# Kernel optimization log

Measured on AMD Instinct MI355X. Metric: run time of the kernel, lower is better.

Reference implementation:

```python
import jax, jax.numpy as jnp
import numpy as np

N = 100000
E = 1600000
D = 128          # in_feat == hidden_size
L = 3            # hidden layers
EPS = 1e-5       # BatchNorm1d eps


def setup_inputs() -> dict:
    key = jax.random.key(0)
    ks = jax.random.split(key, 12)
    x = jax.random.normal(ks[0], (N, D), dtype=jnp.float32)
    edge_index = jax.random.randint(ks[1], (2, E), 0, N, dtype=jnp.int64)
    s = 1.0 / np.sqrt(D)
    # stacked hidden-layer SAGEConv params: lin_l (neighbor), lin_r (root), bias on lin_l
    Wl = jax.random.uniform(ks[2], (L, D, D), jnp.float32, -s, s)
    Wr = jax.random.uniform(ks[3], (L, D, D), jnp.float32, -s, s)
    b = jax.random.uniform(ks[4], (L, D), jnp.float32, -s, s)
    # batchnorm affine params
    gamma = jnp.ones((L, D), jnp.float32)
    beta = jnp.zeros((L, D), jnp.float32)
    # output SAGEConv: D -> 1
    Wl_out = jax.random.uniform(ks[5], (D, 1), jnp.float32, -s, s)
    Wr_out = jax.random.uniform(ks[6], (D, 1), jnp.float32, -s, s)
    b_out = jax.random.uniform(ks[7], (1,), jnp.float32, -s, s)
    return {"x": x, "edge_index": edge_index, "Wl": Wl, "Wr": Wr, "b": b,
            "gamma": gamma, "beta": beta, "Wl_out": Wl_out, "Wr_out": Wr_out,
            "b_out": b_out}


def _sage(x, src, dst, inv_deg, Wl, Wr, b):
    # gather neighbor features along edges, mean-aggregate at destination
    msg_sum = jax.ops.segment_sum(x[src], dst, num_segments=N)   # [N, F]
    mean = msg_sum * inv_deg                                     # 0 for isolated nodes
    return mean @ Wl + x @ Wr + b


def _batchnorm(x, gamma, beta):
    m = jnp.mean(x, axis=0)
    v = jnp.mean((x - m) ** 2, axis=0)  # biased var, as torch BN uses for normalization
    return gamma * (x - m) * jax.lax.rsqrt(v + EPS) + beta


def reference(x, edge_index, Wl, Wr, b, gamma, beta, Wl_out, Wr_out, b_out):
    src, dst = edge_index[0], edge_index[1]
    deg = jax.ops.segment_sum(jnp.ones((E,), x.dtype), dst, num_segments=N)
    inv_deg = jnp.where(deg > 0, 1.0 / jnp.maximum(deg, 1.0), 0.0)[:, None]
    h = x
    for i in range(L):
        h = _sage(h, src, dst, inv_deg, Wl[i], Wr[i], b[i])
        h = jax.nn.relu(h)
        h = _batchnorm(h, gamma[i], beta[i])
    out = _sage(h, src, dst, inv_deg, Wl_out, Wr_out, b_out)
    return jax.nn.sigmoid(out)  # [N, 1]
```

## Files before the change

kernel.cpp:

```cpp
#include <hip/hip_runtime.h>

typedef unsigned short u16;
typedef unsigned int u32;
typedef unsigned long long u64;

#define GN 100000
#define GE 1600000
#define DCAP 64
#define NRANGE 196
#define NBKT (NRANGE * 8)
#define BCAP 1536

typedef __bf16 bf16x8 __attribute__((ext_vector_type(8)));
typedef float f32x4 __attribute__((ext_vector_type(4)));
typedef float f32x2 __attribute__((ext_vector_type(2)));
typedef u32 u32x4 __attribute__((ext_vector_type(4)));
typedef u32 u32x2 __attribute__((ext_vector_type(2)));

__device__ __forceinline__ float bl(u32 u){ return __uint_as_float(u << 16); }
__device__ __forceinline__ float bh(u32 u){ return __uint_as_float(u & 0xffff0000u); }
__device__ __forceinline__ float bfu(u16 v){ return __uint_as_float(((u32)v) << 16); }
__device__ __forceinline__ u16 f2bf(float f){
    u32 u = __float_as_uint(f);
    u32 r = (u + 0x7fffu + ((u >> 16) & 1u)) >> 16;
    return (u16)r;
}
__device__ __forceinline__ u32 pack2(float a, float b){
    return (u32)f2bf(a) | ((u32)f2bf(b) << 16);
}
__device__ __forceinline__ u32 pk8x4(float a, float b, float c, float d){
    u32 p = (u32)__builtin_amdgcn_cvt_pk_fp8_f32(a, b, 0, false);
    p = (u32)__builtin_amdgcn_cvt_pk_fp8_f32(c, d, p, true);
    return p;
}

__global__ void __launch_bounds__(256) k_init(const int* ei, const u32* xraw,
                                              int* cursor, float* colpart, int* flags,
                                              int* bcur){
    int i = blockIdx.x * 256 + threadIdx.x;
    if (i < GN) cursor[i] = 0;
    if (i < NBKT) bcur[i] = 0;
    if (i < 6144) colpart[i] = 0.f;
    int t = threadIdx.x;
    if (blockIdx.x == 0){
        __shared__ int s_any[4];
        int v = 0;
        #pragma unroll
        for (int j = 0; j < 4; ++j){
            int k = t * 4 + j;
            v |= ei[2 * k * 1000 + 1];
        }
        #pragma unroll
        for (int m = 1; m < 64; m <<= 1) v |= __shfl_xor(v, m);
        if ((t & 63) == 0) s_any[t >> 6] = v;
        __syncthreads();
        if (t == 0){
            int any = s_any[0] | s_any[1] | s_any[2] | s_any[3];
            flags[0] = (any == 0) ? 1 : 0;
        }
    }
    if (blockIdx.x == 1){
        __shared__ int s_cnt[4];
        int cnt = 0;
        #pragma unroll
        for (int j = 0; j < 4; ++j){
            int idx = (t * 4 + j) * 6000 + 3;
            u32 u = xraw[idx];
            int e = (u >> 7) & 0xFF;
            cnt += (e >= 100 && e <= 140) ? 1 : 0;
        }
        #pragma unroll
        for (int m = 1; m < 64; m <<= 1) cnt += __shfl_xor(cnt, m);
        if ((t & 63) == 0) s_cnt[t >> 6] = cnt;
        __syncthreads();
        if (t == 0){
            int tot = s_cnt[0] + s_cnt[1] + s_cnt[2] + s_cnt[3];
            flags[1] = (tot > 512) ? 0 : 1;
        }
    }
}

__global__ void __launch_bounds__(256) k_convx(const void* x, const int* flags,
                                               u16* xb, u32* h8){
    int gid = blockIdx.x * 256 + threadIdx.x;
    if (gid >= GN * 16) return;
    float f0,f1,f2,f3,f4,f5,f6,f7;
    if (flags[1]){
        const u32x4* xf = (const u32x4*)x;
        u32x4 a = __builtin_nontemporal_load(xf + gid * 2);
        u32x4 b = __builtin_nontemporal_load(xf + gid * 2 + 1);
        f0 = __uint_as_float(a.x); f1 = __uint_as_float(a.y);
        f2 = __uint_as_float(a.z); f3 = __uint_as_float(a.w);
        f4 = __uint_as_float(b.x); f5 = __uint_as_float(b.y);
        f6 = __uint_as_float(b.z); f7 = __uint_as_float(b.w);
    } else {
        u32x4 g = __builtin_nontemporal_load((const u32x4*)x + gid);
        f0 = bl(g.x); f1 = bh(g.x); f2 = bl(g.y); f3 = bh(g.y);
        f4 = bl(g.z); f5 = bh(g.z); f6 = bl(g.w); f7 = bh(g.w);
    }
    u32x4 o;
    o.x = pack2(f0, f1); o.y = pack2(f2, f3);
    o.z = pack2(f4, f5); o.w = pack2(f6, f7);
    ((u32x4*)xb)[gid] = o;
    u32x2 e = { pk8x4(f0, f1, f2, f3), pk8x4(f4, f5, f6, f7) };
    ((u32x2*)h8)[gid] = e;
}

__global__ void __launch_bounds__(256) k_tofp8(const u16* h, u32* h8){
    int gid = blockIdx.x * 256 + threadIdx.x;
    if (gid >= GN * 16) return;
    u32x4 g = ((const u32x4*)h)[gid];
    u32x2 e = { pk8x4(bl(g.x), bh(g.x), bl(g.y), bh(g.y)),
                pk8x4(bl(g.z), bh(g.z), bl(g.w), bh(g.w)) };
    ((u32x2*)h8)[gid] = e;
}

#define WOFF_WR    49152
#define WOFF_B     98304
#define WOFF_G     98688
#define WOFF_BE    99072
#define WOFF_WLO   99456
#define WOFF_WRO   99584
#define WOFF_BO    99712
#define WTOT       99713
__global__ void __launch_bounds__(256) k_convw(const void* Wl, const void* Wr, const void* b,
                                               const void* g, const void* be, const void* wlo,
                                               const void* wro, const void* bo,
                                               const int* flags, u16* wbuf, float* biasf){
    int i = blockIdx.x * 256 + threadIdx.x;
    if (i >= WTOT) return;
    const void* s; int k;
    if (i < WOFF_B){
        const void* src = (i < WOFF_WR) ? Wl : Wr;
        int r = (i < WOFF_WR) ? i : i - WOFF_WR;
        int layer = r >> 14, L = r & 16383;
        int kk = ((L >> 10) << 3) | (L & 7);
        int cc = (L >> 3) & 127;
        int si = layer * 16384 + kk * 128 + cc;
        float fv = flags[1] ? ((const float*)src)[si] : bfu(((const u16*)src)[si]);
        wbuf[i] = f2bf(fv);
        return;
    }
    if      (i < WOFF_G  ){ s = b;   k = i - WOFF_B; }
    else if (i < WOFF_BE ){ s = g;   k = i - WOFF_G; }
    else if (i < WOFF_WLO){ s = be;  k = i - WOFF_BE; }
    else if (i < WOFF_WRO){ s = wlo; k = i - WOFF_WLO; }
    else if (i < WOFF_BO ){ s = wro; k = i - WOFF_WRO; }
    else                  { s = bo;  k = 0; }
    float fv = flags[1] ? ((const float*)s)[k] : bfu(((const u16*)s)[k]);
    wbuf[i] = f2bf(fv);
    if (i >= WOFF_B && i < WOFF_B + 384) biasf[i - WOFF_B] = fv;
}

__global__ void __launch_bounds__(256) k_fillA(const int* ei, const int* flags,
                                               int* bcur, u64* pairs){
    __shared__ int cnt[256];
    __shared__ int lofs[256];
    __shared__ int gbase[NRANGE];
    __shared__ int wsum[4];
    __shared__ u64 lp[1024];
    int t = threadIdx.x;
    int lane = t & 63, w = t >> 6;
    int res = blockIdx.x & 7;
    int base = blockIdx.x * 1024;
    int is64 = flags[0];
    cnt[t] = 0;
    __syncthreads();
    int myd[4], mys[4], slot[4], myr[4];
    #pragma unroll
    for (int j = 0; j < 4; ++j){
        int e = base + j * 256 + t;
        if (e < GE){
            int d, s;
            if (is64){ d = __builtin_nontemporal_load(ei + 2 * (GE + e));
                       s = __builtin_nontemporal_load(ei + 2 * e); }
            else     { d = __builtin_nontemporal_load(ei + GE + e);
                       s = __builtin_nontemporal_load(ei + e); }
            myd[j] = d; mys[j] = s; myr[j] = d >> 9;
            slot[j] = atomicAdd(&cnt[myr[j]], 1);
        } else myr[j] = -1;
    }
    __syncthreads();
    int v = cnt[t];
    int sv = v;
    #pragma unroll
    for (int d = 1; d < 64; d <<= 1){
        int u = __shfl_up(sv, d);
        if (lane >= d) sv += u;
    }
    if (lane == 63) wsum[w] = sv;
    __syncthreads();
    int prefix = 0;
    #pragma unroll
    for (int j = 0; j < 4; ++j) if (j < w) prefix += wsum[j];
    lofs[t] = sv + prefix - v;
    if (t < NRANGE && cnt[t] > 0)
        gbase[t] = atomicAdd(&bcur[t * 8 + res], cnt[t]);
    __syncthreads();
    #pragma unroll
    for (int j = 0; j < 4; ++j){
        if (myr[j] >= 0)
            lp[lofs[myr[j]] + slot[j]] = ((u64)(u32)myd[j] << 32) | (u32)mys[j];
    }
    __syncthreads();
    int total = GE - base; if (total > 1024) total = 1024;
    for (int i = t; i < total; i += 256){
        u64 pr = lp[i];
        int r = (int)(pr >> 32) >> 9;
        int g = gbase[r] + (i - lofs[r]);
        if (g < BCAP) pairs[((size_t)(r * 8 + res)) * BCAP + g] = pr;
    }
}

__global__ void __launch_bounds__(256) k_fillB(const int* bcur, const u64* pairs,
                                               int* cursor, int* col){
    int range = blockIdx.x % 200;
    int sub   = blockIdx.x / 200;
    if (range >= NRANGE || sub >= 8) return;
    int bkt = range * 8 + sub;
    int n = bcur[bkt]; if (n > BCAP) n = BCAP;
    const u64* P = pairs + (size_t)bkt * BCAP;
    for (int i = threadIdx.x; i < n; i += 256){
        u64 pr = __builtin_nontemporal_load(P + i);
        int s = (int)(u32)pr, d = (int)(pr >> 32);
        int pos = atomicAdd(&cursor[d], 1);
        if (pos < DCAP) col[d * DCAP + pos] = s;
    }
}

__global__ void __launch_bounds__(64) k_agg(const u32* h8, const int* deg, const int* col,
                                            u16* amean){
    int lane = threadIdx.x;
    int grp = lane >> 4;
    int lg  = lane & 15;
    int node = blockIdx.x * 4 + grp;
    if (node >= GN) return;
    int d = deg[node];
    int cnt = d < DCAP ? d : DCAP;
    const int* nb = col + node * DCAP;
    const u32x2* hrow = (const u32x2*)h8;
    f32x2 A01 = {0.f, 0.f}, A23 = {0.f, 0.f}, A45 = {0.f, 0.f}, A67 = {0.f, 0.f};
    int e = 0;
    #define ACC8(v) { \
        A01 += __builtin_amdgcn_cvt_pk_f32_fp8((v).x, false); \
        A23 += __builtin_amdgcn_cvt_pk_f32_fp8((v).x, true);  \
        A45 += __builtin_amdgcn_cvt_pk_f32_fp8((v).y, false); \
        A67 += __builtin_amdgcn_cvt_pk_f32_fp8((v).y, true); }
    for (; e + 7 < cnt; e += 8){
        u32x2 v0 = hrow[(size_t)nb[e]     * 16 + lg];
        u32x2 v1 = hrow[(size_t)nb[e + 1] * 16 + lg];
        u32x2 v2 = hrow[(size_t)nb[e + 2] * 16 + lg];
        u32x2 v3 = hrow[(size_t)nb[e + 3] * 16 + lg];
        u32x2 v4 = hrow[(size_t)nb[e + 4] * 16 + lg];
        u32x2 v5 = hrow[(size_t)nb[e + 5] * 16 + lg];
        u32x2 v6 = hrow[(size_t)nb[e + 6] * 16 + lg];
        u32x2 v7 = hrow[(size_t)nb[e + 7] * 16 + lg];
        ACC8(v0) ACC8(v1) ACC8(v2) ACC8(v3) ACC8(v4) ACC8(v5) ACC8(v6) ACC8(v7)
    }
    for (; e + 1 < cnt; e += 2){
        u32x2 v0 = hrow[(size_t)nb[e]     * 16 + lg];
        u32x2 v1 = hrow[(size_t)nb[e + 1] * 16 + lg];
        ACC8(v0) ACC8(v1)
    }
    if (e < cnt){
        u32x2 v0 = hrow[(size_t)nb[e] * 16 + lg];
        ACC8(v0)
    }
    #undef ACC8
    float inv = (d > 0) ? 1.f / (float)d : 0.f;
    f32x2 iv = {inv, inv};
    A01 *= iv; A23 *= iv; A45 *= iv; A67 *= iv;
    u32x4 o;
    o.x = pack2(A01.x, A01.y);
    o.y = pack2(A23.x, A23.y);
    o.z = pack2(A45.x, A45.y);
    o.w = pack2(A67.x, A67.y);
    ((u32x4*)amean)[(size_t)node * 16 + lg] = o;
}

__global__ void __launch_bounds__(256, 4) k_gemm(const u16* amean, const u16* hin,
                                                 const u16* Wlp, const u16* Wrp,
                                                 const float* biasf,
                                                 u16* hout, float* colpart){
    __shared__ float sst[256];
    int t = threadIdx.x;
    int wid = t >> 6, lane = t & 63;
    int quad = lane >> 4, l15 = lane & 15;
    int r0 = blockIdx.x * 128 + wid * 32;
    int node0 = r0 + l15, node1 = r0 + 16 + l15;
    sst[t] = 0.f;

    f32x4 acc[2][8];
    #pragma unroll
    for (int i = 0; i < 2; i++)
        #pragma unroll
        for (int j = 0; j < 8; j++) acc[i][j] = (f32x4){0.f, 0.f, 0.f, 0.f};

    #pragma unroll
    for (int half = 0; half < 2; ++half){
        const u16* A = half ? hin : amean;
        const u32x4* Wg = (const u32x4*)(half ? Wrp : Wlp);
        #pragma unroll
        for (int s = 0; s < 4; ++s){
            int kk = (s << 5) + (quad << 3);
            union { u32x4 u; bf16x8 v; } fa0, fa1;
            fa0.u = (node0 < GN) ? *(const u32x4*)(A + node0 * 128 + kk) : (u32x4){0,0,0,0};
            fa1.u = (node1 < GN) ? *(const u32x4*)(A + node1 * 128 + kk) : (u32x4){0,0,0,0};
            int kc = (s << 2) + quad;
            const u32x4* wg = Wg + (kc << 7) + l15;
            #pragma unroll
            for (int cb = 0; cb < 8; ++cb){
                union { u32x4 u; bf16x8 v; } fw;
                fw.u = wg[cb << 4];
                acc[0][cb] = __builtin_amdgcn_mfma_f32_16x16x32_bf16(fa0.v, fw.v, acc[0][cb], 0, 0, 0);
                acc[1][cb] = __builtin_amdgcn_mfma_f32_16x16x32_bf16(fa1.v, fw.v, acc[1][cb], 0, 0, 0);
            }
        }
    }
    __syncthreads();

    float bsv[8];
    #pragma unroll
    for (int cb = 0; cb < 8; cb++) bsv[cb] = biasf[cb * 16 + l15];

    #pragma unroll
    for (int cb = 0; cb < 8; cb++){
        float csum = 0.f, csq = 0.f;
        #pragma unroll
        for (int rb = 0; rb < 2; rb++){
            int rbase = r0 + rb * 16 + quad * 4;
            #pragma unroll
            for (int rr = 0; rr < 4; rr++){
                int row = rbase + rr;
                float v = acc[rb][cb][rr] + bsv[cb];
                v = fmaxf(v, 0.f);
                if (row < GN) hout[row * 128 + cb * 16 + l15] = f2bf(v);
                float vm = (row < GN) ? v : 0.f;
                csum += vm; csq += vm * vm;
            }
        }
        csum += __shfl_xor(csum, 16); csum += __shfl_xor(csum, 32);
        csq  += __shfl_xor(csq, 16);  csq  += __shfl_xor(csq, 32);
        if (quad == 0){
            atomicAdd(&sst[cb * 16 + l15], csum);
            atomicAdd(&sst[128 + cb * 16 + l15], csq);
        }
    }
    __syncthreads();
    atomicAdd(&colpart[(blockIdx.x & 7) * 256 + t], sst[t]);
}

__global__ void __launch_bounds__(256) k_bnf(const float* colpart, const u16* gamma, const u16* beta,
                                             int mode,
                                             const u16* WlN, const u16* WrN, u16* wfd,
                                             const float* bNsrc, float* bNdst,
                                             const u16* wlo, const u16* wro, const u16* bo,
                                             u16* hwl, u16* hwr, float* hb){
    __shared__ float s_sc[128], s_sh[128], s_red[256];
    int t = threadIdx.x, b = blockIdx.x;
    if (t < 128){
        float s = 0.f, q = 0.f;
        #pragma unroll
        for (int j = 0; j < 8; ++j){
            s += colpart[j * 256 + t];
            q += colpart[j * 256 + 128 + t];
        }
        const float invn = 1.f / (float)GN;
        float mean = s * invn;
        float var = fmaxf(q * invn - mean * mean, 0.f);
        float rstd = rsqrtf(var + 1e-5f);
        float g  = bfu(gamma[t]);
        float be = bfu(beta[t]);
        float sc = g * rstd, sh = be - mean * sc;
        s_sc[t] = sc; s_sh[t] = sh;
    }
    __syncthreads();
    if (mode == 0){
        if (b < 64){
            int idx = b * 256 + t;
            int k = ((idx >> 10) << 3) | (idx & 7);
            float sc = s_sc[k];
            wfd[idx]         = f2bf(sc * bfu(WlN[idx]));
            wfd[16384 + idx] = f2bf(sc * bfu(WrN[idx]));
        } else if (t < 128){
            float acc = bNsrc[t];
            for (int k = 0; k < 128; ++k){
                int L = ((k >> 3) << 10) + (t << 3) + (k & 7);
                acc += s_sh[k] * (bfu(WlN[L]) + bfu(WrN[L]));
            }
            bNdst[t] = acc;
        }
    } else if (b == 64){
        float contrib = 0.f;
        if (t < 128){
            float wl = bfu(wlo[t]), wr = bfu(wro[t]);
            hwl[t] = f2bf(s_sc[t] * wl);
            hwr[t] = f2bf(s_sc[t] * wr);
            contrib = s_sh[t] * (wl + wr);
        }
        s_red[t] = contrib;
        __syncthreads();
        for (int off = 128; off >= 1; off >>= 1){
            if (t < off) s_red[t] += s_red[t + off];
            __syncthreads();
        }
        if (t == 0) hb[0] = s_red[0] + bfu(bo[0]);
    }
}

__global__ void __launch_bounds__(256) k_dot(const u16* h, const u16* wl, const u16* wr,
                                             float* y, float* r){
    int node = (blockIdx.x * 256 + threadIdx.x) >> 6;
    int lane = threadIdx.x & 63;
    if (node >= GN) return;
    u32 hv  = ((const u32*)h)[node * 64 + lane];
    u32 wlv = ((const u32*)wl)[lane];
    u32 wrv = ((const u32*)wr)[lane];
    float hlo = bl(hv), hhi = bh(hv);
    float ya = hlo * bl(wlv) + hhi * bh(wlv);
    float ra = hlo * bl(wrv) + hhi * bh(wrv);
    #pragma unroll
    for (int m = 1; m < 64; m <<= 1){ ya += __shfl_xor(ya, m); ra += __shfl_xor(ra, m); }
    if (lane == 0){ y[node] = ya; r[node] = ra; }
}

__global__ void __launch_bounds__(256) k_out(const float* y, const float* r, const int* deg,
                                             const int* col, const float* hb,
                                             const int* flags, void* out){
    int n = blockIdx.x * 256 + threadIdx.x;
    if (n >= GN) return;
    int d = deg[n];
    int cnt = d < DCAP ? d : DCAP;
    const int* nb = col + n * DCAP;
    float s = 0.f;
    for (int e = 0; e < cnt; ++e) s += y[nb[e]];
    float inv = (d > 0) ? 1.f / (float)d : 0.f;
    float z = inv * s + r[n] + hb[0];
    float sg = 1.f / (1.f + __expf(-z));
    if (flags[1]) ((float*)out)[n] = sg;
    else          ((u16*)out)[n] = f2bf(sg);
}

extern "C" void kernel_launch(void* const* d_in, const int* in_sizes, int n_in,
                              void* d_out, int out_size, void* d_ws, size_t ws_size,
                              hipStream_t stream) {
    const void* x     = d_in[0];
    const int*  ei    = (const int*)d_in[1];
    const void* Wl    = d_in[2];
    const void* Wr    = d_in[3];
    const void* bias  = d_in[4];
    const void* gamma = d_in[5];
    const void* beta  = d_in[6];
    const void* wlout = d_in[7];
    const void* wrout = d_in[8];
    const void* bout  = d_in[9];

    char* p = (char*)d_ws;
    auto take = [&](size_t b){ void* q = (void*)p; p += (b + 255) & ~(size_t)255; return q; };
    int*   cursor = (int*)  take((size_t)GN * 4);
    int*   flags  = (int*)  take(256);
    int*   bcur   = (int*)  take((size_t)NBKT * 4);
    float* colpart= (float*)take(6144 * 4);
    float* biasf  = (float*)take(384 * 4);
    float* bf2    = (float*)take(128 * 4);
    float* bf3    = (float*)take(128 * 4);
    float* hb     = (float*)take(256);
    u16*   wf2    = (u16*)  take(32768 * 2);
    u16*   wf3    = (u16*)  take(32768 * 2);
    u16*   hwl    = (u16*)  take(128 * 2);
    u16*   hwr    = (u16*)  take(128 * 2);
    float* yv     = (float*)take((size_t)GN * 4);
    float* rv     = (float*)take((size_t)GN * 4);
    int*   col    = (int*)  take((size_t)GN * DCAP * 4);
    u16*   xb     = (u16*)  take((size_t)GN * 128 * 2);
    u16*   amean  = (u16*)  take((size_t)GN * 128 * 2);
    u16*   hbuf   = (u16*)  take((size_t)GN * 128 * 2);
    u32*   h8     = (u32*)  take((size_t)GN * 128);
    u16*   wbuf   = (u16*)  take((size_t)WTOT * 2);

    u64* pairs = (u64*)amean;

    const int NB_N = (GN + 255) / 256;
    const int NB_A4 = (GN + 3) / 4;
    const int NB_W = (GN + 3) / 4;
    const int NB_G = (GN + 127) / 128;
    const int NB_M = (GN * 16 + 255) / 256;
    const int NB_C = (WTOT + 255) / 256;
    const int NB_A = (GE + 1023) / 1024;

    k_init <<<NB_N, 256, 0, stream>>>(ei, (const u32*)x, cursor, colpart, flags, bcur);
    k_convx<<<NB_M, 256, 0, stream>>>(x, flags, xb, h8);
    k_convw<<<NB_C, 256, 0, stream>>>(Wl, Wr, bias, gamma, beta, wlout, wrout, bout, flags, wbuf, biasf);
    k_fillA<<<NB_A, 256, 0, stream>>>(ei, flags, bcur, pairs);
    k_fillB<<<1600, 256, 0, stream>>>(bcur, pairs, cursor, col);

    const u16* hin = xb;
    for (int i = 0; i < 3; ++i){
        const u16* Wlp; const u16* Wrp; const float* bfi;
        if (i == 0){ Wlp = wbuf;     Wrp = wbuf + WOFF_WR; bfi = biasf; }
        else if (i == 1){ Wlp = wf2; Wrp = wf2 + 16384;    bfi = bf2; }
        else { Wlp = wf3;            Wrp = wf3 + 16384;    bfi = bf3; }
        u16* wfd = (i == 0) ? wf2 : wf3;
        float* bNdst = (i == 0) ? bf2 : bf3;
        int nx = (i < 2) ? (i + 1) : 0;
        k_agg <<<NB_A4, 64, 0, stream>>>(h8, cursor, col, amean);
        k_gemm<<<NB_G, 256, 0, stream>>>(amean, hin, Wlp, Wrp, bfi, hbuf,
                                         colpart + i * 2048);
        k_bnf <<<65, 256, 0, stream>>>(colpart + i * 2048,
            wbuf + WOFF_G + i * 128, wbuf + WOFF_BE + i * 128, (i == 2) ? 1 : 0,
            wbuf + nx * 16384, wbuf + WOFF_WR + nx * 16384, wfd,
            biasf + nx * 128, bNdst,
            wbuf + WOFF_WLO, wbuf + WOFF_WRO, wbuf + WOFF_BO, hwl, hwr, hb);
        if (i < 2) k_tofp8<<<NB_M, 256, 0, stream>>>(hbuf, h8);
        hin = hbuf;
    }
    k_dot<<<NB_W, 256, 0, stream>>>(hbuf, hwl, hwr, yv, rv);
    k_out<<<NB_N, 256, 0, stream>>>(yv, rv, cursor, col, hb, flags, d_out);
}
```

Measured before the change: 448.6 us.

## Merge input conversion kernels, widen aggregation blocks, preload GEMM A fragments

Merges the x conversion and weight conversion kernels into one launch split by block index, removing one kernel launch. The aggregation kernel now runs two wavefronts per block (8 nodes) instead of one. The GEMM kernel loads all A-operand fragments for both halves up front before the MFMA loop, and its launch bound drops from 4 to 2 blocks per CU to make room for the extra registers, which may lower occupancy.

```diff
diff --git a/kernel.cpp b/kernel.cpp
--- a/kernel.cpp
+++ b/kernel.cpp
@@ -10,6 +10,8 @@
 #define NRANGE 196
 #define NBKT (NRANGE * 8)
 #define BCAP 1536
+#define NBM 6250
+#define NBC 390
 
 typedef __bf16 bf16x8 __attribute__((ext_vector_type(8)));
 typedef float f32x4 __attribute__((ext_vector_type(4)));
@@ -80,41 +82,6 @@
     }
 }
 
-__global__ void __launch_bounds__(256) k_convx(const void* x, const int* flags,
-                                               u16* xb, u32* h8){
-    int gid = blockIdx.x * 256 + threadIdx.x;
-    if (gid >= GN * 16) return;
-    float f0,f1,f2,f3,f4,f5,f6,f7;
-    if (flags[1]){
-        const u32x4* xf = (const u32x4*)x;
-        u32x4 a = __builtin_nontemporal_load(xf + gid * 2);
-        u32x4 b = __builtin_nontemporal_load(xf + gid * 2 + 1);
-        f0 = __uint_as_float(a.x); f1 = __uint_as_float(a.y);
-        f2 = __uint_as_float(a.z); f3 = __uint_as_float(a.w);
-        f4 = __uint_as_float(b.x); f5 = __uint_as_float(b.y);
-        f6 = __uint_as_float(b.z); f7 = __uint_as_float(b.w);
-    } else {
-        u32x4 g = __builtin_nontemporal_load((const u32x4*)x + gid);
-        f0 = bl(g.x); f1 = bh(g.x); f2 = bl(g.y); f3 = bh(g.y);
-        f4 = bl(g.z); f5 = bh(g.z); f6 = bl(g.w); f7 = bh(g.w);
-    }
-    u32x4 o;
-    o.x = pack2(f0, f1); o.y = pack2(f2, f3);
-    o.z = pack2(f4, f5); o.w = pack2(f6, f7);
-    ((u32x4*)xb)[gid] = o;
-    u32x2 e = { pk8x4(f0, f1, f2, f3), pk8x4(f4, f5, f6, f7) };
-    ((u32x2*)h8)[gid] = e;
-}
-
-__global__ void __launch_bounds__(256) k_tofp8(const u16* h, u32* h8){
-    int gid = blockIdx.x * 256 + threadIdx.x;
-    if (gid >= GN * 16) return;
-    u32x4 g = ((const u32x4*)h)[gid];
-    u32x2 e = { pk8x4(bl(g.x), bh(g.x), bl(g.y), bh(g.y)),
-                pk8x4(bl(g.z), bh(g.z), bl(g.w), bh(g.w)) };
-    ((u32x2*)h8)[gid] = e;
-}
-
 #define WOFF_WR    49152
 #define WOFF_B     98304
 #define WOFF_G     98688
@@ -123,11 +90,38 @@
 #define WOFF_WRO   99584
 #define WOFF_BO    99712
 #define WTOT       99713
-__global__ void __launch_bounds__(256) k_convw(const void* Wl, const void* Wr, const void* b,
-                                               const void* g, const void* be, const void* wlo,
-                                               const void* wro, const void* bo,
-                                               const int* flags, u16* wbuf, float* biasf){
-    int i = blockIdx.x * 256 + threadIdx.x;
+__global__ void __launch_bounds__(256) k_conv(const void* x, const void* Wl, const void* Wr,
+                                              const void* b, const void* g, const void* be,
+                                              const void* wlo, const void* wro, const void* bo,
+                                              const int* flags, u16* xb, u32* h8,
+                                              u16* wbuf, float* biasf){
+    int t = threadIdx.x;
+    if (blockIdx.x < NBM){
+        int gid = blockIdx.x * 256 + t;
+        if (gid >= GN * 16) return;
+        float f0,f1,f2,f3,f4,f5,f6,f7;
+        if (flags[1]){
+            const u32x4* xf = (const u32x4*)x;
+            u32x4 a = __builtin_nontemporal_load(xf + gid * 2);
+            u32x4 c = __builtin_nontemporal_load(xf + gid * 2 + 1);
+            f0 = __uint_as_float(a.x); f1 = __uint_as_float(a.y);
+            f2 = __uint_as_float(a.z); f3 = __uint_as_float(a.w);
+            f4 = __uint_as_float(c.x); f5 = __uint_as_float(c.y);
+            f6 = __uint_as_float(c.z); f7 = __uint_as_float(c.w);
+        } else {
+            u32x4 gg = __builtin_nontemporal_load((const u32x4*)x + gid);
+            f0 = bl(gg.x); f1 = bh(gg.x); f2 = bl(gg.y); f3 = bh(gg.y);
+            f4 = bl(gg.z); f5 = bh(gg.z); f6 = bl(gg.w); f7 = bh(gg.w);
+        }
+        u32x4 o;
+        o.x = pack2(f0, f1); o.y = pack2(f2, f3);
+        o.z = pack2(f4, f5); o.w = pack2(f6, f7);
+        ((u32x4*)xb)[gid] = o;
+        u32x2 e = { pk8x4(f0, f1, f2, f3), pk8x4(f4, f5, f6, f7) };
+        ((u32x2*)h8)[gid] = e;
+        return;
+    }
+    int i = (blockIdx.x - NBM) * 256 + t;
     if (i >= WTOT) return;
     const void* s; int k;
     if (i < WOFF_B){
@@ -150,6 +144,15 @@
     float fv = flags[1] ? ((const float*)s)[k] : bfu(((const u16*)s)[k]);
     wbuf[i] = f2bf(fv);
     if (i >= WOFF_B && i < WOFF_B + 384) biasf[i - WOFF_B] = fv;
+}
+
+__global__ void __launch_bounds__(256) k_tofp8(const u16* h, u32* h8){
+    int gid = blockIdx.x * 256 + threadIdx.x;
+    if (gid >= GN * 16) return;
+    u32x4 g = ((const u32x4*)h)[gid];
+    u32x2 e = { pk8x4(bl(g.x), bh(g.x), bl(g.y), bh(g.y)),
+                pk8x4(bl(g.z), bh(g.z), bl(g.w), bh(g.w)) };
+    ((u32x2*)h8)[gid] = e;
 }
 
 __global__ void __launch_bounds__(256) k_fillA(const int* ei, const int* flags,
@@ -228,12 +231,13 @@
     }
 }
 
-__global__ void __launch_bounds__(64) k_agg(const u32* h8, const int* deg, const int* col,
-                                            u16* amean){
-    int lane = threadIdx.x;
+__global__ void __launch_bounds__(128) k_agg(const u32* h8, const int* deg, const int* col,
+                                             u16* amean){
+    int t = threadIdx.x;
+    int wid = t >> 6, lane = t & 63;
     int grp = lane >> 4;
     int lg  = lane & 15;
-    int node = blockIdx.x * 4 + grp;
+    int node = blockIdx.x * 8 + wid * 4 + grp;
     if (node >= GN) return;
     int d = deg[node];
     int cnt = d < DCAP ? d : DCAP;
@@ -278,7 +282,7 @@
     ((u32x4*)amean)[(size_t)node * 16 + lg] = o;
 }
 
-__global__ void __launch_bounds__(256, 4) k_gemm(const u16* amean, const u16* hin,
+__global__ void __launch_bounds__(256, 2) k_gemm(const u16* amean, const u16* hin,
                                                  const u16* Wlp, const u16* Wrp,
                                                  const float* biasf,
                                                  u16* hout, float* colpart){
@@ -290,30 +294,37 @@
     int node0 = r0 + l15, node1 = r0 + 16 + l15;
     sst[t] = 0.f;
 
-    f32x4 acc[2][8];
-    #pragma unroll
-    for (int i = 0; i < 2; i++)
-        #pragma unroll
-        for (int j = 0; j < 8; j++) acc[i][j] = (f32x4){0.f, 0.f, 0.f, 0.f};
-
+    union { u32x4 u; bf16x8 v; } fa[2][2][4];
     #pragma unroll
     for (int half = 0; half < 2; ++half){
         const u16* A = half ? hin : amean;
-        const u32x4* Wg = (const u32x4*)(half ? Wrp : Wlp);
         #pragma unroll
         for (int s = 0; s < 4; ++s){
             int kk = (s << 5) + (quad << 3);
-            union { u32x4 u; bf16x8 v; } fa0, fa1;
-            fa0.u = (node0 < GN) ? *(const u32x4*)(A + node0 * 128 + kk) : (u32x4){0,0,0,0};
-            fa1.u = (node1 < GN) ? *(const u32x4*)(A + node1 * 128 + kk) : (u32x4){0,0,0,0};
+            fa[half][0][s].u = (node0 < GN) ? *(const u32x4*)(A + node0 * 128 + kk) : (u32x4){0,0,0,0};
+            fa[half][1][s].u = (node1 < GN) ? *(const u32x4*)(A + node1 * 128 + kk) : (u32x4){0,0,0,0};
+        }
+    }
+
+    f32x4 acc[2][8];
+    #pragma unroll
+    for (int i = 0; i < 2; i++)
+        #pragma unroll
+        for (int j = 0; j < 8; j++) acc[i][j] = (f32x4){0.f, 0.f, 0.f, 0.f};
+
+    #pragma unroll
+    for (int half = 0; half < 2; ++half){
+        const u32x4* Wg = (const u32x4*)(half ? Wrp : Wlp);
+        #pragma unroll
+        for (int s = 0; s < 4; ++s){
             int kc = (s << 2) + quad;
             const u32x4* wg = Wg + (kc << 7) + l15;
             #pragma unroll
             for (int cb = 0; cb < 8; ++cb){
                 union { u32x4 u; bf16x8 v; } fw;
                 fw.u = wg[cb << 4];
-                acc[0][cb] = __builtin_amdgcn_mfma_f32_16x16x32_bf16(fa0.v, fw.v, acc[0][cb], 0, 0, 0);
-                acc[1][cb] = __builtin_amdgcn_mfma_f32_16x16x32_bf16(fa1.v, fw.v, acc[1][cb], 0, 0, 0);
+                acc[0][cb] = __builtin_amdgcn_mfma_f32_16x16x32_bf16(fa[half][0][s].v, fw.v, acc[0][cb], 0, 0, 0);
+                acc[1][cb] = __builtin_amdgcn_mfma_f32_16x16x32_bf16(fa[half][1][s].v, fw.v, acc[1][cb], 0, 0, 0);
             }
         }
     }
@@ -481,16 +492,15 @@
     u64* pairs = (u64*)amean;
 
     const int NB_N = (GN + 255) / 256;
-    const int NB_A4 = (GN + 3) / 4;
+    const int NB_A8 = (GN + 7) / 8;
     const int NB_W = (GN + 3) / 4;
     const int NB_G = (GN + 127) / 128;
     const int NB_M = (GN * 16 + 255) / 256;
-    const int NB_C = (WTOT + 255) / 256;
     const int NB_A = (GE + 1023) / 1024;
 
     k_init <<<NB_N, 256, 0, stream>>>(ei, (const u32*)x, cursor, colpart, flags, bcur);
-    k_convx<<<NB_M, 256, 0, stream>>>(x, flags, xb, h8);
-    k_convw<<<NB_C, 256, 0, stream>>>(Wl, Wr, bias, gamma, beta, wlout, wrout, bout, flags, wbuf, biasf);
+    k_conv <<<NBM + NBC, 256, 0, stream>>>(x, Wl, Wr, bias, gamma, beta, wlout, wrout, bout,
+                                           flags, xb, h8, wbuf, biasf);
     k_fillA<<<NB_A, 256, 0, stream>>>(ei, flags, bcur, pairs);
     k_fillB<<<1600, 256, 0, stream>>>(bcur, pairs, cursor, col);
 
@@ -503,7 +513,7 @@
         u16* wfd = (i == 0) ? wf2 : wf3;
         float* bNdst = (i == 0) ? bf2 : bf3;
         int nx = (i < 2) ? (i + 1) : 0;
-        k_agg <<<NB_A4, 64, 0, stream>>>(h8, cursor, col, amean);
+        k_agg <<<NB_A8, 128, 0, stream>>>(h8, cursor, col, amean);
         k_gemm<<<NB_G, 256, 0, stream>>>(amean, hin, Wlp, Wrp, bfi, hbuf,
                                          colpart + i * 2048);
         k_bnf <<<65, 256, 0, stream>>>(colpart + i * 2048,
```

Result: slower. 465.4 us (+3.7%).
